# Kernel optimization log

Measured on AMD Instinct MI355X. Metric: run time of the kernel, lower is better.

## Reference

```python
import jax, jax.numpy as jnp
import numpy as np

B, LQ, LK = 4, 256, 512
DQ = DK = PROJ = 256


def setup_inputs() -> dict:
    key = jax.random.key(0)
    ks = jax.random.split(key, 8)
    query = jax.random.normal(ks[0], (B, LQ, DQ), dtype=jnp.float32)
    keys = jax.random.normal(ks[1], (B, LK, DK), dtype=jnp.float32)
    attn_mask = jax.random.bernoulli(ks[2], 0.1, (B, LQ, LK))
    # Linear(query_size+key_size, proj) split into query/key halves (same math as concat @ W1)
    s1 = 1.0 / np.sqrt(DQ + DK)
    Wq = jax.random.uniform(ks[3], (DQ, PROJ), jnp.float32, -s1, s1)
    Wk = jax.random.uniform(ks[4], (DK, PROJ), jnp.float32, -s1, s1)
    b1 = jax.random.uniform(ks[5], (PROJ,), jnp.float32, -s1, s1)
    s2 = 1.0 / np.sqrt(PROJ)
    w2 = jax.random.uniform(ks[6], (PROJ,), jnp.float32, -s2, s2)
    b2 = jax.random.uniform(ks[7], (), jnp.float32, -s2, s2)
    return {"query": query, "keys": keys, "attn_mask": attn_mask,
            "Wq": Wq, "Wk": Wk, "b1": b1, "w2": w2, "b2": b2}


def reference(query, keys, attn_mask, Wq, Wk, b1, w2, b2):
    # cat(q_expand, k_expand) @ W1 == q@Wq broadcast-added to k@Wk (avoids the huge concat)
    qp = jnp.einsum('bqd,dp->bqp', query, Wq)            # (B,Lq,P)
    kp = jnp.einsum('bkd,dp->bkp', keys, Wk)             # (B,Lk,P)
    h = jnp.tanh(qp[:, :, None, :] + kp[:, None, :, :] + b1)  # (B,Lq,Lk,P)
    logits = jnp.einsum('bqkp,p->bqk', h, w2) + b2        # (B,Lq,Lk)
    logits = jnp.where(attn_mask, -jnp.inf, logits)
    return logits
```

## Files before the change

kernel.cpp:

```cpp
#include <hip/hip_runtime.h>
#include <math.h>

#define B_ 4
#define LQ_ 256
#define LK_ 512
#define D_ 256
#define P_ 256

#define SC 2.8853900817779268f

#define MASK_SENTINEL (-3.0e38f)

__global__ __launch_bounds__(256) void proj_kernel(
    const float* __restrict__ Q, const float* __restrict__ Kx,
    const float* __restrict__ Wq, const float* __restrict__ Wk,
    const float* __restrict__ b1,
    float* __restrict__ Eq, float* __restrict__ Ek)
{
    __shared__ __align__(16) float Ws[256][68];

    const int bm = blockIdx.x;
    const int bn = blockIdx.y;
    const bool isq = (bm < 32);
    const int m0 = isq ? bm * 32 : (bm - 32) * 32;
    const float* A = isq ? Q : Kx;
    const float* W = isq ? Wq : Wk;
    float* outp    = isq ? Eq : Ek;
    const int n0 = bn * 64;

    const int t  = threadIdx.x;
    const int tx = t & 15;
    const int ty = t >> 4;

    #pragma unroll
    for (int i = 0; i < 16; ++i) {
        int f  = t + i * 256;
        int r  = f >> 4;
        int c4 = (f & 15) * 4;
        *(float4*)&Ws[r][c4] = *(const float4*)&W[(size_t)r * P_ + n0 + c4];
    }
    __syncthreads();

    const float* arow0 = A + (size_t)(m0 + ty) * D_;
    const float* arow1 = A + (size_t)(m0 + ty + 16) * D_;

    float acc[2][4] = {};

    float4 a0c = *(const float4*)&arow0[0];
    float4 a1c = *(const float4*)&arow1[0];
    float4 w0c = *(const float4*)&Ws[0][tx * 4];
    float4 w1c = *(const float4*)&Ws[1][tx * 4];
    float4 w2c = *(const float4*)&Ws[2][tx * 4];
    float4 w3c = *(const float4*)&Ws[3][tx * 4];

    #pragma unroll 4
    for (int k4 = 0; k4 < 64; ++k4) {
        float4 a0 = a0c, a1 = a1c, w0 = w0c, w1 = w1c, w2v = w2c, w3 = w3c;
        if (k4 < 63) {
            a0c = *(const float4*)&arow0[(k4 + 1) * 4];
            a1c = *(const float4*)&arow1[(k4 + 1) * 4];
            w0c = *(const float4*)&Ws[k4 * 4 + 4][tx * 4];
            w1c = *(const float4*)&Ws[k4 * 4 + 5][tx * 4];
            w2c = *(const float4*)&Ws[k4 * 4 + 6][tx * 4];
            w3c = *(const float4*)&Ws[k4 * 4 + 7][tx * 4];
        }
        float av[2][4] = {{a0.x,a0.y,a0.z,a0.w},{a1.x,a1.y,a1.z,a1.w}};
        float wv[4][4] = {{w0.x,w0.y,w0.z,w0.w},{w1.x,w1.y,w1.z,w1.w},
                          {w2v.x,w2v.y,w2v.z,w2v.w},{w3.x,w3.y,w3.z,w3.w}};
        #pragma unroll
        for (int kk = 0; kk < 4; ++kk)
            #pragma unroll
            for (int i = 0; i < 2; ++i)
                #pragma unroll
                for (int j = 0; j < 4; ++j)
                    acc[i][j] = fmaf(av[i][kk], wv[kk][j], acc[i][j]);
    }

    float bv[4] = {0.f, 0.f, 0.f, 0.f};
    if (!isq) {
        float4 b = *(const float4*)&b1[n0 + tx * 4];
        bv[0] = b.x; bv[1] = b.y; bv[2] = b.z; bv[3] = b.w;
    }

    #pragma unroll
    for (int i = 0; i < 2; ++i) {
        int m = m0 + ty + i * 16;
        float4 o;
        o.x = __builtin_amdgcn_exp2f(SC * (acc[i][0] + bv[0]));
        o.y = __builtin_amdgcn_exp2f(SC * (acc[i][1] + bv[1]));
        o.z = __builtin_amdgcn_exp2f(SC * (acc[i][2] + bv[2]));
        o.w = __builtin_amdgcn_exp2f(SC * (acc[i][3] + bv[3]));
        *(float4*)&outp[(size_t)m * P_ + n0 + tx * 4] = o;
    }
}

__global__ __launch_bounds__(256, 4) void logits_kernel(
    const float* __restrict__ Eq, const float* __restrict__ Ek,
    const unsigned char* __restrict__ mask,
    const float* __restrict__ w2, const float* __restrict__ b2,
    float* __restrict__ out)
{
    __shared__ __align__(16) float eqs[32][132];
    __shared__ __align__(16) float eks[32][132];
    __shared__ float partial[4];

    const int b  = blockIdx.z;
    const int q0 = blockIdx.y * 32;
    const int k0 = blockIdx.x * 32;
    const int t  = threadIdx.x;

    const int tx = t & 15;
    const int ty = t >> 4;

    size_t oidx[2][2];
    unsigned char mb[2][2];
    #pragma unroll
    for (int i = 0; i < 2; ++i)
        #pragma unroll
        for (int j = 0; j < 2; ++j) {
            oidx[i][j] = (size_t)(b * LQ_ + q0 + ty + i * 16) * LK_ + (k0 + tx + j * 16);
            mb[i][j] = mask[oidx[i][j]];
        }

    float wv = w2[t];
    #pragma unroll
    for (int s = 32; s > 0; s >>= 1) wv += __shfl_xor(wv, s);
    if ((t & 63) == 0) partial[t >> 6] = wv;

    float acc[2][2] = {};

    for (int pc = 0; pc < 2; ++pc) {
        __syncthreads();
        const int p0 = pc * 128;
        #pragma unroll
        for (int i = 0; i < 2; ++i) {
            int f = t + i * 256;
            int r = f >> 5;
            int c = (f & 31) * 4;
            *(float4*)&eqs[r][c] = *(const float4*)&Eq[(size_t)(b * LQ_ + q0 + r) * P_ + p0 + c];
            *(float4*)&eks[r][c] = *(const float4*)&Ek[(size_t)(b * LK_ + k0 + r) * P_ + p0 + c];
        }
        __syncthreads();

        const float* q0p = &eqs[ty][0];
        const float* q1p = &eqs[ty + 16][0];
        const float* k0p = &eks[tx][0];
        const float* k1p = &eks[tx + 16][0];
        const float* wp  = w2 + p0;

        #pragma unroll 4
        for (int p4 = 0; p4 < 32; ++p4) {
            const float4 w = *(const float4*)&wp[p4 * 4];
            float4 qv[2], kv[2];
            qv[0] = *(const float4*)(q0p + p4 * 4);
            qv[1] = *(const float4*)(q1p + p4 * 4);
            kv[0] = *(const float4*)(k0p + p4 * 4);
            kv[1] = *(const float4*)(k1p + p4 * 4);
            float qa[2][4] = {{qv[0].x,qv[0].y,qv[0].z,qv[0].w},
                              {qv[1].x,qv[1].y,qv[1].z,qv[1].w}};
            float ka[2][4] = {{kv[0].x,kv[0].y,kv[0].z,kv[0].w},
                              {kv[1].x,kv[1].y,kv[1].z,kv[1].w}};
            #pragma unroll
            for (int i = 0; i < 2; ++i)
                #pragma unroll
                for (int j = 0; j < 2; ++j) {
                    float x0 = fmaf(qa[i][0], ka[j][0], 1.f);
                    float x1 = fmaf(qa[i][1], ka[j][1], 1.f);
                    float x2 = fmaf(qa[i][2], ka[j][2], 1.f);
                    float x3 = fmaf(qa[i][3], ka[j][3], 1.f);
                    float d01 = x0 * x1;
                    float d23 = x2 * x3;
                    float n01 = fmaf(w.x, x1, w.y * x0);
                    float n23 = fmaf(w.z, x3, w.w * x2);
                    acc[i][j] = fmaf(fmaf(n01, d23, n23 * d01),
                                     __builtin_amdgcn_rcpf(d01 * d23),
                                     acc[i][j]);
                }
        }
    }

    const float base = partial[0] + partial[1] + partial[2] + partial[3] + b2[0];

    #pragma unroll
    for (int i = 0; i < 2; ++i)
        #pragma unroll
        for (int j = 0; j < 2; ++j)
            out[oidx[i][j]] = mb[i][j] ? MASK_SENTINEL : fmaf(-2.f, acc[i][j], base);
}

extern "C" void kernel_launch(void* const* d_in, const int* in_sizes, int n_in,
                              void* d_out, int out_size, void* d_ws, size_t ws_size,
                              hipStream_t stream) {
    const float* query        = (const float*)d_in[0];
    const float* keys         = (const float*)d_in[1];
    const unsigned char* mask = (const unsigned char*)d_in[2];
    const float* Wq           = (const float*)d_in[3];
    const float* Wk           = (const float*)d_in[4];
    const float* b1           = (const float*)d_in[5];
    const float* w2           = (const float*)d_in[6];
    const float* b2           = (const float*)d_in[7];
    float* out = (float*)d_out;

    float* Eq = (float*)d_ws;
    float* Ek = Eq + (size_t)B_ * LQ_ * P_;

    dim3 g1(96, 4);
    proj_kernel<<<g1, 256, 0, stream>>>(query, keys, Wq, Wk, b1, Eq, Ek);

    dim3 g2(LK_ / 32, LQ_ / 32, B_);
    logits_kernel<<<g2, 256, 0, stream>>>(Eq, Ek, mask, w2, b2, out);
}
```

Measured before the change: 32.08 us.

## Split logits reduction over P into two halves with separate combine kernel

Splits the P=256 reduction in the logits kernel across two grid slices, so twice as many blocks each handle 128 projection dims, and writes the partial sums to workspace. A new combine kernel adds the two partials, applies bias and mask with vectorized loads, and writes the output. The aim is more parallelism and better occupancy across the GPU's compute units, in exchange for an extra kernel launch and an extra round trip of partial logits through memory.

```diff
diff --git a/kernel.cpp b/kernel.cpp
--- a/kernel.cpp
+++ b/kernel.cpp
@@ -94,98 +94,107 @@
     }
 }
 
-__global__ __launch_bounds__(256, 4) void logits_kernel(
+__global__ __launch_bounds__(256, 4) void logits_partial_kernel(
     const float* __restrict__ Eq, const float* __restrict__ Ek,
-    const unsigned char* __restrict__ mask,
+    const float* __restrict__ w2, float* __restrict__ part)
+{
+    __shared__ __align__(16) float eqs[32][132];
+    __shared__ __align__(16) float eks[32][132];
+
+    const int kt = blockIdx.x;
+    const int qt = blockIdx.y;
+    const int zz = blockIdx.z;
+    const int b  = zz >> 1;
+    const int ph = zz & 1;
+    const int q0 = qt * 32, k0 = kt * 32, p0 = ph * 128;
+    const int t  = threadIdx.x;
+    const int tx = t & 15;
+    const int ty = t >> 4;
+
+    #pragma unroll
+    for (int i = 0; i < 4; ++i) {
+        int f = t + i * 256;
+        int r = f >> 5;
+        int c = (f & 31) * 4;
+        *(float4*)&eqs[r][c] = *(const float4*)&Eq[(size_t)(b * LQ_ + q0 + r) * P_ + p0 + c];
+        *(float4*)&eks[r][c] = *(const float4*)&Ek[(size_t)(b * LK_ + k0 + r) * P_ + p0 + c];
+    }
+    __syncthreads();
+
+    const float* q0p = &eqs[ty][0];
+    const float* q1p = &eqs[ty + 16][0];
+    const float* k0p = &eks[tx][0];
+    const float* k1p = &eks[tx + 16][0];
+    const float* wp  = w2 + p0;
+
+    float acc[2][2] = {};
+
+    #pragma unroll 4
+    for (int p4 = 0; p4 < 32; ++p4) {
+        const float4 w = *(const float4*)&wp[p4 * 4];
+        float4 qv[2], kv[2];
+        qv[0] = *(const float4*)(q0p + p4 * 4);
+        qv[1] = *(const float4*)(q1p + p4 * 4);
+        kv[0] = *(const float4*)(k0p + p4 * 4);
+        kv[1] = *(const float4*)(k1p + p4 * 4);
+        float qa[2][4] = {{qv[0].x,qv[0].y,qv[0].z,qv[0].w},
+                          {qv[1].x,qv[1].y,qv[1].z,qv[1].w}};
+        float ka[2][4] = {{kv[0].x,kv[0].y,kv[0].z,kv[0].w},
+                          {kv[1].x,kv[1].y,kv[1].z,kv[1].w}};
+        #pragma unroll
+        for (int i = 0; i < 2; ++i)
+            #pragma unroll
+            for (int j = 0; j < 2; ++j) {
+                float x0 = fmaf(qa[i][0], ka[j][0], 1.f);
+                float x1 = fmaf(qa[i][1], ka[j][1], 1.f);
+                float x2 = fmaf(qa[i][2], ka[j][2], 1.f);
+                float x3 = fmaf(qa[i][3], ka[j][3], 1.f);
+                float d01 = x0 * x1;
+                float d23 = x2 * x3;
+                float n01 = fmaf(w.x, x1, w.y * x0);
+                float n23 = fmaf(w.z, x3, w.w * x2);
+                acc[i][j] = fmaf(fmaf(n01, d23, n23 * d01),
+                                 __builtin_amdgcn_rcpf(d01 * d23),
+                                 acc[i][j]);
+            }
+    }
+
+    float* pp = part + (size_t)ph * ((size_t)B_ * LQ_ * LK_);
+    #pragma unroll
+    for (int i = 0; i < 2; ++i)
+        #pragma unroll
+        for (int j = 0; j < 2; ++j)
+            pp[(size_t)(b * LQ_ + q0 + ty + i * 16) * LK_ + (k0 + tx + j * 16)] = acc[i][j];
+}
+
+__global__ __launch_bounds__(256) void combine_kernel(
+    const float* __restrict__ part, const unsigned char* __restrict__ mask,
     const float* __restrict__ w2, const float* __restrict__ b2,
     float* __restrict__ out)
 {
-    __shared__ __align__(16) float eqs[32][132];
-    __shared__ __align__(16) float eks[32][132];
-    __shared__ float partial[4];
-
-    const int b  = blockIdx.z;
-    const int q0 = blockIdx.y * 32;
-    const int k0 = blockIdx.x * 32;
-    const int t  = threadIdx.x;
-
-    const int tx = t & 15;
-    const int ty = t >> 4;
-
-    size_t oidx[2][2];
-    unsigned char mb[2][2];
-    #pragma unroll
-    for (int i = 0; i < 2; ++i)
-        #pragma unroll
-        for (int j = 0; j < 2; ++j) {
-            oidx[i][j] = (size_t)(b * LQ_ + q0 + ty + i * 16) * LK_ + (k0 + tx + j * 16);
-            mb[i][j] = mask[oidx[i][j]];
-        }
+    __shared__ float ps[4];
+    const int t = threadIdx.x;
 
     float wv = w2[t];
     #pragma unroll
     for (int s = 32; s > 0; s >>= 1) wv += __shfl_xor(wv, s);
-    if ((t & 63) == 0) partial[t >> 6] = wv;
-
-    float acc[2][2] = {};
-
-    for (int pc = 0; pc < 2; ++pc) {
-        __syncthreads();
-        const int p0 = pc * 128;
-        #pragma unroll
-        for (int i = 0; i < 2; ++i) {
-            int f = t + i * 256;
-            int r = f >> 5;
-            int c = (f & 31) * 4;
-            *(float4*)&eqs[r][c] = *(const float4*)&Eq[(size_t)(b * LQ_ + q0 + r) * P_ + p0 + c];
-            *(float4*)&eks[r][c] = *(const float4*)&Ek[(size_t)(b * LK_ + k0 + r) * P_ + p0 + c];
-        }
-        __syncthreads();
-
-        const float* q0p = &eqs[ty][0];
-        const float* q1p = &eqs[ty + 16][0];
-        const float* k0p = &eks[tx][0];
-        const float* k1p = &eks[tx + 16][0];
-        const float* wp  = w2 + p0;
-
-        #pragma unroll 4
-        for (int p4 = 0; p4 < 32; ++p4) {
-            const float4 w = *(const float4*)&wp[p4 * 4];
-            float4 qv[2], kv[2];
-            qv[0] = *(const float4*)(q0p + p4 * 4);
-            qv[1] = *(const float4*)(q1p + p4 * 4);
-            kv[0] = *(const float4*)(k0p + p4 * 4);
-            kv[1] = *(const float4*)(k1p + p4 * 4);
-            float qa[2][4] = {{qv[0].x,qv[0].y,qv[0].z,qv[0].w},
-                              {qv[1].x,qv[1].y,qv[1].z,qv[1].w}};
-            float ka[2][4] = {{kv[0].x,kv[0].y,kv[0].z,kv[0].w},
-                              {kv[1].x,kv[1].y,kv[1].z,kv[1].w}};
-            #pragma unroll
-            for (int i = 0; i < 2; ++i)
-                #pragma unroll
-                for (int j = 0; j < 2; ++j) {
-                    float x0 = fmaf(qa[i][0], ka[j][0], 1.f);
-                    float x1 = fmaf(qa[i][1], ka[j][1], 1.f);
-                    float x2 = fmaf(qa[i][2], ka[j][2], 1.f);
-                    float x3 = fmaf(qa[i][3], ka[j][3], 1.f);
-                    float d01 = x0 * x1;
-                    float d23 = x2 * x3;
-                    float n01 = fmaf(w.x, x1, w.y * x0);
-                    float n23 = fmaf(w.z, x3, w.w * x2);
-                    acc[i][j] = fmaf(fmaf(n01, d23, n23 * d01),
-                                     __builtin_amdgcn_rcpf(d01 * d23),
-                                     acc[i][j]);
-                }
-        }
-    }
-
-    const float base = partial[0] + partial[1] + partial[2] + partial[3] + b2[0];
-
-    #pragma unroll
-    for (int i = 0; i < 2; ++i)
-        #pragma unroll
-        for (int j = 0; j < 2; ++j)
-            out[oidx[i][j]] = mb[i][j] ? MASK_SENTINEL : fmaf(-2.f, acc[i][j], base);
+    if ((t & 63) == 0) ps[t >> 6] = wv;
+    __syncthreads();
+    const float base = ps[0] + ps[1] + ps[2] + ps[3] + b2[0];
+
+    const size_t idx4 = (size_t)blockIdx.x * 256 + t;
+    const size_t STR4 = (size_t)B_ * LQ_ * LK_ / 4;
+
+    const float4 s0 = ((const float4*)part)[idx4];
+    const float4 s1 = ((const float4*)part)[idx4 + STR4];
+    const unsigned int mb = ((const unsigned int*)mask)[idx4];
+
+    float4 o;
+    o.x = (mb & 0x000000ffu) ? MASK_SENTINEL : fmaf(-2.f, s0.x + s1.x, base);
+    o.y = (mb & 0x0000ff00u) ? MASK_SENTINEL : fmaf(-2.f, s0.y + s1.y, base);
+    o.z = (mb & 0x00ff0000u) ? MASK_SENTINEL : fmaf(-2.f, s0.z + s1.z, base);
+    o.w = (mb & 0xff000000u) ? MASK_SENTINEL : fmaf(-2.f, s0.w + s1.w, base);
+    ((float4*)out)[idx4] = o;
 }
 
 extern "C" void kernel_launch(void* const* d_in, const int* in_sizes, int n_in,
@@ -201,12 +210,15 @@
     const float* b2           = (const float*)d_in[7];
     float* out = (float*)d_out;
 
-    float* Eq = (float*)d_ws;
-    float* Ek = Eq + (size_t)B_ * LQ_ * P_;
+    float* Eq   = (float*)d_ws;
+    float* Ek   = Eq + (size_t)B_ * LQ_ * P_;
+    float* part = Ek + (size_t)B_ * LK_ * P_;
 
     dim3 g1(96, 4);
     proj_kernel<<<g1, 256, 0, stream>>>(query, keys, Wq, Wk, b1, Eq, Ek);
 
-    dim3 g2(LK_ / 32, LQ_ / 32, B_);
-    logits_kernel<<<g2, 256, 0, stream>>>(Eq, Ek, mask, w2, b2, out);
-}
+    dim3 g2(LK_ / 32, LQ_ / 32, B_ * 2);
+    logits_partial_kernel<<<g2, 256, 0, stream>>>(Eq, Ek, w2, part);
+
+    combine_kernel<<<512, 256, 0, stream>>>(part, mask, w2, b2, out);
+}
```

After: 36.05 us. 1.12x slower.
